# Kernel optimization log

Measured on AMD Instinct MI355X. Metric: run time of the kernel, lower is better.

Reference implementation:

```python
import jax, jax.numpy as jnp
import numpy as np
from jax import lax

XI = 2.0
RADIUS = int(3 * XI)  # 6 -> kernel size 13


def _gaussian_weight(xi: float):
    radius = int(3 * xi)
    coords = jnp.arange(-radius, radius + 1, dtype=jnp.float32)
    g1 = jnp.exp(-coords ** 2 / (2.0 * xi * xi))
    g1 = g1 / g1.sum()
    g3 = g1[:, None, None] * g1[None, :, None] * g1[None, None, :]  # (K,K,K)
    # grouped conv weight: (out_ch=3, in_ch/groups=1, K, K, K), same kernel per channel
    return jnp.broadcast_to(g3[None, None], (3, 1) + g3.shape)


def setup_inputs() -> dict:
    key = jax.random.key(0)
    x = jax.random.normal(key, (1, 3, 192, 192, 192), dtype=jnp.float32)
    w = _gaussian_weight(XI)
    return {"x": x, "w": w}


def reference(x, w):
    # depthwise (groups=3) 3D cross-correlation with 'same' padding = radius,
    # matching nn.Conv3d(3, 3, (K,K,K), padding=radius, groups=3, bias=False)
    r = (w.shape[-1] - 1) // 2
    return lax.conv_general_dilated(
        x, w,
        window_strides=(1, 1, 1),
        padding=[(r, r)] * 3,
        dimension_numbers=("NCDHW", "OIDHW", "NCDHW"),
        feature_group_count=3,
    )
```

## Files before the change

### kernel.cpp

```cpp
#include <hip/hip_runtime.h>

#define RAD 6
#define KS 13
#define DIM 192
#define CH 3
#define W4C 48
#define PLANE4 (DIM * W4C)
#define VOL4 (DIM * PLANE4)
#define VOL (DIM * DIM * DIM)
#define TOTAL (CH * VOL)

__global__ void g1_extract_kernel(const float* __restrict__ w, float* __restrict__ g1) {
    int i = threadIdx.x;
    if (i < KS) {
        float s = 0.f;
        for (int j = 0; j < KS * KS; ++j) s += w[i * KS * KS + j];
        g1[i] = s;
    }
}

#define HT 64
#define HL (HT + 2 * RAD)
#define NLD (HL * W4C)

__global__ __launch_bounds__(256) void conv_wh_kernel(const float* __restrict__ in,
                                                      float* __restrict__ out,
                                                      const float* __restrict__ g1) {
    __shared__ float4 tile[NLD];
    const int bid = blockIdx.x;
    const int ht = bid % 3;
    const int d = (bid / 3) % DIM;
    const int c = bid / (3 * DIM);
    const int h0 = ht * HT;
    const int t = threadIdx.x;

    float g[KS];
#pragma unroll
    for (int k = 0; k < KS; ++k) g[k] = g1[k];

    const float4* in4 = (const float4*)in;
    float4* out4 = (float4*)out;
    const size_t plane = (size_t)c * VOL4 + (size_t)d * PLANE4;
    const float4 z4 = make_float4(0.f, 0.f, 0.f, 0.f);

#pragma unroll
    for (int i = 0; i < 15; ++i) {
        int idx = t + i * 256;
        if (idx < NLD) {
            int h = h0 - RAD + idx / W4C;
            tile[idx] = (h >= 0 && h < DIM) ? in4[plane + (size_t)h * W4C + (idx % W4C)] : z4;
        }
    }
    __syncthreads();

    float4 va[15];
#pragma unroll
    for (int i = 0; i < 15; ++i) {
        int idx = t + i * 256;
        if (idx < NLD) {
            int row = idx / W4C, w4 = idx % W4C;
            int w0 = w4 * 4;
            float f[20];
#pragma unroll
            for (int b = 0; b < 5; ++b) {
                int j = min(max(w4 + b - 2, 0), W4C - 1);
                float4 v = tile[row * W4C + j];
                f[4 * b + 0] = v.x; f[4 * b + 1] = v.y;
                f[4 * b + 2] = v.z; f[4 * b + 3] = v.w;
            }
#pragma unroll
            for (int j = 0; j < 20; ++j) {
                int ww = w0 - 8 + j;
                if (ww < 0 || ww >= DIM) f[j] = 0.f;
            }
            float4 o = z4;
#pragma unroll
            for (int k = 0; k < KS; ++k) {
                o.x += g[k] * f[k + 2];
                o.y += g[k] * f[k + 3];
                o.z += g[k] * f[k + 4];
                o.w += g[k] * f[k + 5];
            }
            va[i] = o;
        }
    }
    __syncthreads();
#pragma unroll
    for (int i = 0; i < 15; ++i) {
        int idx = t + i * 256;
        if (idx < NLD) tile[idx] = va[i];
    }
    __syncthreads();

    if (t < 192) {
        int w4 = t % W4C;
        int seg = t / W4C;
        int hh0 = seg * 16;

        float4 buf[KS];
#pragma unroll
        for (int j = 0; j < KS; ++j) buf[j] = tile[(hh0 + j) * W4C + w4];

#pragma unroll
        for (int i = 0; i < 16; ++i) {
            float4 a = z4;
#pragma unroll
            for (int j = 0; j < KS; ++j) {
                const float4 v = buf[(i + j) % KS];
                float gw = g[j];
                a.x += gw * v.x; a.y += gw * v.y; a.z += gw * v.z; a.w += gw * v.w;
            }
            out4[plane + (size_t)(h0 + hh0 + i) * W4C + w4] = a;
            if (i < 15) buf[i % KS] = tile[(hh0 + i + KS) * W4C + w4];
        }
    }
}

#define WT 16

__global__ __launch_bounds__(256) void conv_d_kernel(const float* __restrict__ in,
                                                     float* __restrict__ out,
                                                     const float* __restrict__ g1) {
    __shared__ float4 tile[DIM * WT];
    const int bid = blockIdx.x;
    const int wt = bid % 3;
    const int h = (bid / 3) % DIM;
    const int c = bid / (3 * DIM);
    const int t = threadIdx.x;

    float g[KS];
#pragma unroll
    for (int k = 0; k < KS; ++k) g[k] = g1[k];

    const float4* in4 = (const float4*)in;
    float4* out4 = (float4*)out;
    const size_t base = (size_t)c * VOL4 + (size_t)h * W4C + wt * WT;
    const float4 z4 = make_float4(0.f, 0.f, 0.f, 0.f);

#pragma unroll
    for (int i = 0; i < 12; ++i) {
        int idx = t + i * 256;
        int dd = idx / WT, w = idx % WT;
        tile[idx] = in4[base + (size_t)dd * PLANE4 + w];
    }
    __syncthreads();

    int w = t % WT;
    int seg = t / WT;
    int d0 = seg * 12;

    float4 buf[KS];
#pragma unroll
    for (int j = 0; j < KS; ++j) {
        int dd = d0 - RAD + j;
        buf[j] = (dd >= 0 && dd < DIM) ? tile[dd * WT + w] : z4;
    }

#pragma unroll
    for (int i = 0; i < 12; ++i) {
        float4 a = z4;
#pragma unroll
        for (int j = 0; j < KS; ++j) {
            const float4 v = buf[(i + j) % KS];
            float gw = g[j];
            a.x += gw * v.x; a.y += gw * v.y; a.z += gw * v.z; a.w += gw * v.w;
        }
        out4[base + (size_t)(d0 + i) * PLANE4 + w] = a;
        if (i < 11) {
            int dl = d0 + i + RAD + 1;
            buf[i % KS] = (dl < DIM) ? tile[dl * WT + w] : z4;
        }
    }
}

__global__ void naive_conv3d_kernel(const float* __restrict__ x, const float* __restrict__ w,
                                    float* __restrict__ out, int total) {
    int n = blockIdx.x * blockDim.x + threadIdx.x;
    if (n >= total) return;
    int wp = n % DIM;
    int h = (n / DIM) % DIM;
    int d = (n / (DIM * DIM)) % DIM;
    int c = n / (DIM * DIM * DIM);
    const float* wc = w + c * KS * KS * KS;
    const float* xc = x + (size_t)c * DIM * DIM * DIM;
    float acc = 0.f;
    for (int kd = 0; kd < KS; ++kd) {
        int dd = d + kd - RAD;
        if (dd < 0 || dd >= DIM) continue;
        for (int kh = 0; kh < KS; ++kh) {
            int hh = h + kh - RAD;
            if (hh < 0 || hh >= DIM) continue;
            for (int kw = 0; kw < KS; ++kw) {
                int ww = wp + kw - RAD;
                if (ww < 0 || ww >= DIM) continue;
                acc += wc[(kd * KS + kh) * KS + kw] * xc[((size_t)dd * DIM + hh) * DIM + ww];
            }
        }
    }
    out[n] = acc;
}

extern "C" void kernel_launch(void* const* d_in, const int* in_sizes, int n_in,
                              void* d_out, int out_size, void* d_ws, size_t ws_size,
                              hipStream_t stream) {
    const float* x = (const float*)d_in[0];
    const float* w = (const float*)d_in[1];
    float* out = (float*)d_out;

    const size_t inter_bytes = (size_t)TOTAL * sizeof(float);

    if (ws_size >= inter_bytes + 64) {
        float* inter = (float*)d_ws;
        float* g1 = (float*)((char*)d_ws + inter_bytes);

        g1_extract_kernel<<<1, 64, 0, stream>>>(w, g1);

        conv_wh_kernel<<<CH * DIM * 3, 256, 0, stream>>>(x, inter, g1);

        conv_d_kernel<<<CH * DIM * 3, 256, 0, stream>>>(inter, out, g1);
    } else {
        const int threads = 256;
        const int blocks = (TOTAL + threads - 1) / threads;
        naive_conv3d_kernel<<<blocks, threads, 0, stream>>>(x, w, out, TOTAL);
    }
}
```

Before: 213.7 us.

## Split fused W/H pass into three separable 1D passes with padded LDS tiles

Replaces the fused W+H kernel with a W-only kernel that writes to the output buffer, then runs a templated 1D axis kernel for H (into the workspace) and D (back into the output). The H and D passes share one kernel whose LDS rows are padded to 17 float4 to reduce bank conflicts. This removes the halo-row recompute and the large LDS tile of the fused kernel, at the cost of an extra full-volume read and write pass through global memory.

```diff
diff --git a/kernel.cpp b/kernel.cpp
--- a/kernel.cpp
+++ b/kernel.cpp
@@ -19,141 +19,101 @@
     }
 }
 
-#define HT 64
-#define HL (HT + 2 * RAD)
-#define NLD (HL * W4C)
+__global__ __launch_bounds__(256) void conv_w_lds(const float* __restrict__ in,
+                                                  float* __restrict__ out,
+                                                  const float* __restrict__ g1) {
+    __shared__ float4 tile[768];
+    const int bid = blockIdx.x;
+    const int rt = bid % 12;
+    const int d = (bid / 12) % DIM;
+    const int c = bid / (12 * DIM);
+    const int t = threadIdx.x;
+    const size_t base4 = (size_t)c * VOL4 + (size_t)d * PLANE4 + (size_t)(rt * 16) * W4C;
 
-__global__ __launch_bounds__(256) void conv_wh_kernel(const float* __restrict__ in,
-                                                      float* __restrict__ out,
-                                                      const float* __restrict__ g1) {
-    __shared__ float4 tile[NLD];
-    const int bid = blockIdx.x;
-    const int ht = bid % 3;
-    const int d = (bid / 3) % DIM;
-    const int c = bid / (3 * DIM);
-    const int h0 = ht * HT;
-    const int t = threadIdx.x;
+    const float4* in4 = (const float4*)in;
+    float4* out4 = (float4*)out;
 
     float g[KS];
 #pragma unroll
     for (int k = 0; k < KS; ++k) g[k] = g1[k];
 
-    const float4* in4 = (const float4*)in;
-    float4* out4 = (float4*)out;
-    const size_t plane = (size_t)c * VOL4 + (size_t)d * PLANE4;
-    const float4 z4 = make_float4(0.f, 0.f, 0.f, 0.f);
-
 #pragma unroll
-    for (int i = 0; i < 15; ++i) {
+    for (int i = 0; i < 3; ++i) {
         int idx = t + i * 256;
-        if (idx < NLD) {
-            int h = h0 - RAD + idx / W4C;
-            tile[idx] = (h >= 0 && h < DIM) ? in4[plane + (size_t)h * W4C + (idx % W4C)] : z4;
-        }
+        tile[idx] = in4[base4 + idx];
     }
     __syncthreads();
 
-    float4 va[15];
 #pragma unroll
-    for (int i = 0; i < 15; ++i) {
+    for (int i = 0; i < 3; ++i) {
         int idx = t + i * 256;
-        if (idx < NLD) {
-            int row = idx / W4C, w4 = idx % W4C;
-            int w0 = w4 * 4;
-            float f[20];
+        int row = idx / W4C, w4 = idx % W4C;
+        int w0 = w4 * 4;
+        float f[20];
 #pragma unroll
-            for (int b = 0; b < 5; ++b) {
-                int j = min(max(w4 + b - 2, 0), W4C - 1);
-                float4 v = tile[row * W4C + j];
-                f[4 * b + 0] = v.x; f[4 * b + 1] = v.y;
-                f[4 * b + 2] = v.z; f[4 * b + 3] = v.w;
-            }
+        for (int b = 0; b < 5; ++b) {
+            int j = min(max(w4 + b - 2, 0), W4C - 1);
+            float4 v = tile[row * W4C + j];
+            f[4 * b + 0] = v.x; f[4 * b + 1] = v.y;
+            f[4 * b + 2] = v.z; f[4 * b + 3] = v.w;
+        }
 #pragma unroll
-            for (int j = 0; j < 20; ++j) {
-                int ww = w0 - 8 + j;
-                if (ww < 0 || ww >= DIM) f[j] = 0.f;
-            }
-            float4 o = z4;
+        for (int j = 0; j < 20; ++j) {
+            int ww = w0 - 8 + j;
+            if (ww < 0 || ww >= DIM) f[j] = 0.f;
+        }
+        float4 o = make_float4(0.f, 0.f, 0.f, 0.f);
 #pragma unroll
-            for (int k = 0; k < KS; ++k) {
-                o.x += g[k] * f[k + 2];
-                o.y += g[k] * f[k + 3];
-                o.z += g[k] * f[k + 4];
-                o.w += g[k] * f[k + 5];
-            }
-            va[i] = o;
+        for (int k = 0; k < KS; ++k) {
+            o.x += g[k] * f[k + 2];
+            o.y += g[k] * f[k + 3];
+            o.z += g[k] * f[k + 4];
+            o.w += g[k] * f[k + 5];
         }
-    }
-    __syncthreads();
-#pragma unroll
-    for (int i = 0; i < 15; ++i) {
-        int idx = t + i * 256;
-        if (idx < NLD) tile[idx] = va[i];
-    }
-    __syncthreads();
-
-    if (t < 192) {
-        int w4 = t % W4C;
-        int seg = t / W4C;
-        int hh0 = seg * 16;
-
-        float4 buf[KS];
-#pragma unroll
-        for (int j = 0; j < KS; ++j) buf[j] = tile[(hh0 + j) * W4C + w4];
-
-#pragma unroll
-        for (int i = 0; i < 16; ++i) {
-            float4 a = z4;
-#pragma unroll
-            for (int j = 0; j < KS; ++j) {
-                const float4 v = buf[(i + j) % KS];
-                float gw = g[j];
-                a.x += gw * v.x; a.y += gw * v.y; a.z += gw * v.z; a.w += gw * v.w;
-            }
-            out4[plane + (size_t)(h0 + hh0 + i) * W4C + w4] = a;
-            if (i < 15) buf[i % KS] = tile[(hh0 + i + KS) * W4C + w4];
-        }
+        out4[base4 + idx] = o;
     }
 }
 
-#define WT 16
+#define LPAD 17
 
-__global__ __launch_bounds__(256) void conv_d_kernel(const float* __restrict__ in,
+template <int AXS>
+__global__ __launch_bounds__(256) void conv_axis_lds(const float* __restrict__ in,
                                                      float* __restrict__ out,
                                                      const float* __restrict__ g1) {
-    __shared__ float4 tile[DIM * WT];
+    __shared__ float4 tile[DIM * LPAD];
     const int bid = blockIdx.x;
     const int wt = bid % 3;
-    const int h = (bid / 3) % DIM;
+    const int other = (bid / 3) % DIM;
     const int c = bid / (3 * DIM);
     const int t = threadIdx.x;
+    const size_t ostride = (AXS == W4C) ? (size_t)PLANE4 : (size_t)W4C;
+    const size_t base4 = (size_t)c * VOL4 + (size_t)other * ostride + (size_t)(wt * 16);
+
+    const float4* in4 = (const float4*)in;
+    float4* out4 = (float4*)out;
 
     float g[KS];
 #pragma unroll
     for (int k = 0; k < KS; ++k) g[k] = g1[k];
 
-    const float4* in4 = (const float4*)in;
-    float4* out4 = (float4*)out;
-    const size_t base = (size_t)c * VOL4 + (size_t)h * W4C + wt * WT;
-    const float4 z4 = make_float4(0.f, 0.f, 0.f, 0.f);
-
 #pragma unroll
     for (int i = 0; i < 12; ++i) {
         int idx = t + i * 256;
-        int dd = idx / WT, w = idx % WT;
-        tile[idx] = in4[base + (size_t)dd * PLANE4 + w];
+        int p = idx / 16, w = idx % 16;
+        tile[p * LPAD + w] = in4[base4 + (size_t)p * AXS + w];
     }
     __syncthreads();
 
-    int w = t % WT;
-    int seg = t / WT;
-    int d0 = seg * 12;
+    const int w = t % 16;
+    const int seg = t / 16;
+    const int p0 = seg * 12;
+    const float4 z4 = make_float4(0.f, 0.f, 0.f, 0.f);
 
     float4 buf[KS];
 #pragma unroll
     for (int j = 0; j < KS; ++j) {
-        int dd = d0 - RAD + j;
-        buf[j] = (dd >= 0 && dd < DIM) ? tile[dd * WT + w] : z4;
+        int p = p0 - RAD + j;
+        buf[j] = (p >= 0 && p < DIM) ? tile[p * LPAD + w] : z4;
     }
 
 #pragma unroll
@@ -165,10 +125,10 @@
             float gw = g[j];
             a.x += gw * v.x; a.y += gw * v.y; a.z += gw * v.z; a.w += gw * v.w;
         }
-        out4[base + (size_t)(d0 + i) * PLANE4 + w] = a;
+        out4[base4 + (size_t)(p0 + i) * AXS + w] = a;
         if (i < 11) {
-            int dl = d0 + i + RAD + 1;
-            buf[i % KS] = (dl < DIM) ? tile[dl * WT + w] : z4;
+            int pl = p0 + i + RAD + 1;
+            buf[i % KS] = (pl < DIM) ? tile[pl * LPAD + w] : z4;
         }
     }
 }
@@ -215,9 +175,11 @@
 
         g1_extract_kernel<<<1, 64, 0, stream>>>(w, g1);
 
-        conv_wh_kernel<<<CH * DIM * 3, 256, 0, stream>>>(x, inter, g1);
+        conv_w_lds<<<CH * DIM * 12, 256, 0, stream>>>(x, out, g1);
 
-        conv_d_kernel<<<CH * DIM * 3, 256, 0, stream>>>(inter, out, g1);
+        conv_axis_lds<W4C><<<CH * DIM * 3, 256, 0, stream>>>(out, inter, g1);
+
+        conv_axis_lds<PLANE4><<<CH * DIM * 3, 256, 0, stream>>>(inter, out, g1);
     } else {
         const int threads = 256;
         const int blocks = (TOTAL + threads - 1) / threads;
```

After: 210.7 us. About the same (-1.4%).
